# Optimization experiments

Hardware: AMD Instinct MI355X
Metric: run time of the kernel (lower is better)

## Reference

```python
import jax, jax.numpy as jnp
import numpy as np

B, S, T = 1024, 1024, 16


def setup_inputs() -> dict:
    key = jax.random.key(0)
    k1, k2, k3, k4, k5 = jax.random.split(key, 5)
    emissions = jax.random.normal(k1, (B, S, T), dtype=jnp.float32)
    tags = jax.random.randint(k2, (B, S), 0, T, dtype=jnp.int64)
    mask = jnp.ones((B, S), dtype=bool)
    # parameters (original uses uniform(-0.1, 0.1) init)
    transitions = jax.random.uniform(k3, (T, T), minval=-0.1, maxval=0.1, dtype=jnp.float32)
    start_transitions = jax.random.uniform(k4, (T,), minval=-0.1, maxval=0.1, dtype=jnp.float32)
    end_transitions = jax.random.uniform(k5, (T,), minval=-0.1, maxval=0.1, dtype=jnp.float32)
    return {
        "emissions": emissions,
        "tags": tags,
        "mask": mask,
        "transitions": transitions,
        "start_transitions": start_transitions,
        "end_transitions": end_transitions,
    }


def _forward_algorithm(emissions, mask, transitions, start_transitions, end_transitions):
    # emissions: [B,S,T], mask: [B,S] bool -> log partition [B]
    score0 = start_transitions + emissions[:, 0]  # [B,T]

    def step(score, xs):
        em_t, m_t = xs  # em_t: [B,T], m_t: [B]
        # next[b,i,j] = score[b,i] + transitions[i,j] + em_t[b,j]
        nxt = score[:, :, None] + transitions[None, :, :] + em_t[:, None, :]
        nxt = jax.nn.logsumexp(nxt, axis=1)  # over previous tag i
        score = jnp.where(m_t[:, None], nxt, score)
        return score, None

    em_rest = jnp.swapaxes(emissions[:, 1:], 0, 1)  # [S-1,B,T]
    m_rest = jnp.swapaxes(mask[:, 1:], 0, 1)        # [S-1,B]
    score, _ = jax.lax.scan(step, score0, (em_rest, m_rest))
    score = score + end_transitions
    return jax.nn.logsumexp(score, axis=1)


def _score_sentence(emissions, tags, mask, transitions, start_transitions, end_transitions):
    # gold-path score, vectorized over time. [B]
    bidx = jnp.arange(emissions.shape[0])
    score = start_transitions[tags[:, 0]] + emissions[:, 0][bidx, tags[:, 0]]
    # per-step emission scores [B,S]
    emit = jnp.take_along_axis(emissions, tags[:, :, None], axis=2)[:, :, 0]
    # NOTE: faithful to original: transitions[tags[t], tags[t-1]]
    trans = transitions[tags[:, 1:], tags[:, :-1]]  # [B,S-1]
    m = mask[:, 1:].astype(emissions.dtype)
    score = score + jnp.sum((emit[:, 1:] + trans) * m, axis=1)
    last_idx = jnp.sum(mask.astype(jnp.int32), axis=1) - 1  # [B]
    last_tags = jnp.take_along_axis(tags, last_idx[:, None].astype(tags.dtype), axis=1)[:, 0]
    score = score + end_transitions[last_tags]
    return score


def reference(emissions, tags, mask, transitions, start_transitions, end_transitions):
    emissions = emissions.astype(jnp.float32)
    gold = _score_sentence(emissions, tags, mask, transitions, start_transitions, end_transitions)
    logZ = _forward_algorithm(emissions, mask, transitions, start_transitions, end_transitions)
    nll = logZ - gold
    return jnp.mean(nll)
```

## Files before the change

kernel.cpp:

```cpp
#include <hip/hip_runtime.h>
#include <stdint.h>


#define BB 1024
#define SS 1024
#define TT 16
#define CC 16
#define LL 64
#define P1B (BB * CC / 4)

typedef float    f32x4 __attribute__((ext_vector_type(4)));
typedef int      i32x4 __attribute__((ext_vector_type(4)));
typedef short    s16x4 __attribute__((ext_vector_type(4)));
typedef uint32_t u32x2 __attribute__((ext_vector_type(2)));

__device__ __forceinline__ uint32_t pkt(float lo, float hi) {
    return __builtin_amdgcn_perm(__float_as_uint(hi), __float_as_uint(lo), 0x07060302u);
}
__device__ __forceinline__ s16x4 mk_frag(uint32_t lo, uint32_t hi) {
    u32x2 t; t.x = lo; t.y = hi;
    return __builtin_bit_cast(s16x4, t);
}

__global__ __launch_bounds__(256, 4) void fused1_kernel(
        const float* __restrict__ em,
        const float* __restrict__ trans,
        const int*   __restrict__ tags,
        const float* __restrict__ startt,
        const float* __restrict__ endt,
        float* __restrict__ mats,
        int*   __restrict__ scales,
        float* __restrict__ gold)
{
    __shared__ float xbuf[4][LL * TT];
    __shared__ int   sbuf[4][16];
    __shared__ float red[256];
    if (blockIdx.x < P1B) {
        const int wave = threadIdx.x >> 6;
        const int lane = threadIdx.x & 63;
        const int id   = blockIdx.x * 4 + wave;
        const int b    = id >> 4;
        const int c    = id & 15;
        const int q    = lane >> 4;
        const int m    = lane & 15;

        const float comp = 1.00390625f;
        const float a0 = __expf(trans[(4*q + 0) * TT + m]) * comp;
        const float a1 = __expf(trans[(4*q + 1) * TT + m]) * comp;
        const float a2 = __expf(trans[(4*q + 2) * TT + m]) * comp;
        const float a3 = __expf(trans[(4*q + 3) * TT + m]) * comp;
        const s16x4 afr = mk_frag(pkt(a0, a1), pkt(a2, a3));

        const float* ep = em + (size_t)b * SS * TT + (size_t)c * LL * TT + lane;
        float* xb = xbuf[wave];
        {
            float v[16];
            #pragma unroll
            for (int k = 0; k < 16; ++k) v[k] = ep[k * 64];
            #pragma unroll
            for (int k = 0; k < 16; ++k) xb[k * 64 + lane] = __expf(v[k]);
        }

        f32x4 sd0, sd1;
        sd0[0] = sd1[0] = (4*q + 0 == m) ? 1.f : 0.f;
        sd0[1] = sd1[1] = (4*q + 1 == m) ? 1.f : 0.f;
        sd0[2] = sd1[2] = (4*q + 2 == m) ? 1.f : 0.f;
        sd0[3] = sd1[3] = (4*q + 3 == m) ? 1.f : 0.f;
        const f32x4 zero = {0.f, 0.f, 0.f, 0.f};
        int sc0 = 0, sc1 = 0;
        const bool skip0 = (c == 0);

#define RESCALE(sd, sc) {                                                   \
        float mx = fmaxf(fmaxf(sd[0], sd[1]), fmaxf(sd[2], sd[3]));         \
        mx = fmaxf(mx, __shfl_xor(mx, 16, 64));                             \
        mx = fmaxf(mx, __shfl_xor(mx, 32, 64));                             \
        const int e_ = (int)(__float_as_uint(mx) >> 23) - 127;              \
        const float sf_ = __uint_as_float((uint32_t)(127 - e_) << 23);      \
        sd[0] *= sf_; sd[1] *= sf_; sd[2] *= sf_; sd[3] *= sf_;             \
        sc += e_; }

        const float* xlo = xb + 4 * q;
        const float* xhi = xb + 512 + 4 * q;
        f32x4 x0 = *(const f32x4*)(xlo);
        f32x4 x1 = *(const f32x4*)(xhi);

        #pragma unroll
        for (int i = 0; i < 32; ++i) {
            f32x4 nx0, nx1;
            if (i < 31) {
                nx0 = *(const f32x4*)(xlo + (i + 1) * TT);
                nx1 = *(const f32x4*)(xhi + (i + 1) * TT);
            }
            if (!(skip0 && i == 0)) {
                const s16x4 b0 = mk_frag(pkt(sd0[0], sd0[1]), pkt(sd0[2], sd0[3]));
                const f32x4 d0 = __builtin_amdgcn_mfma_f32_16x16x16bf16_1k(afr, b0, zero, 0, 0, 0);
                sd0 = d0 * x0;
            }
            {
                const s16x4 b1 = mk_frag(pkt(sd1[0], sd1[1]), pkt(sd1[2], sd1[3]));
                const f32x4 d1 = __builtin_amdgcn_mfma_f32_16x16x16bf16_1k(afr, b1, zero, 0, 0, 0);
                sd1 = d1 * x1;
            }
            x0 = nx0; x1 = nx1;
            if ((i & 7) == 7) { RESCALE(sd0, sc0); RESCALE(sd1, sc1); }
        }

        xb[(4*q + 0) * TT + m] = sd1[0];
        xb[(4*q + 1) * TT + m] = sd1[1];
        xb[(4*q + 2) * TT + m] = sd1[2];
        xb[(4*q + 3) * TT + m] = sd1[3];
        if (q == 0) sbuf[wave][m] = sc1;
        const f32x4 at  = *(const f32x4*)(xb + m * TT + 4 * q);
        const i32x4 sh  = *(const i32x4*)(sbuf[wave] + 4 * q);
        int shimax = sc1;
        #pragma unroll
        for (int s = 1; s < 16; s <<= 1) shimax = max(shimax, __shfl_xor(shimax, s, 64));
        const float r0 = ldexpf(sd0[0], sh.x - shimax);
        const float r1 = ldexpf(sd0[1], sh.y - shimax);
        const float r2 = ldexpf(sd0[2], sh.z - shimax);
        const float r3 = ldexpf(sd0[3], sh.w - shimax);
        const s16x4 bfm = mk_frag(pkt(r0, r1), pkt(r2, r3));
        const s16x4 afm = mk_frag(pkt(at.x, at.y), pkt(at.z, at.w));
        f32x4 sd = __builtin_amdgcn_mfma_f32_16x16x16bf16_1k(afm, bfm, zero, 0, 0, 0);
        int sc = sc0 + shimax;
        RESCALE(sd, sc);
#undef RESCALE

        float* mp = mats + (size_t)id * 256;
        mp[(4*q + 0) * TT + m] = sd[0];
        mp[(4*q + 1) * TT + m] = sd[1];
        mp[(4*q + 2) * TT + m] = sd[2];
        mp[(4*q + 3) * TT + m] = sd[3];
        if (q == 0) scales[id * 16 + m] = sc;
    } else {
        const int b = blockIdx.x - P1B, tid = threadIdx.x;
        float local = 0.f;
        for (int t = tid; t < SS; t += 256) {
            const int tg = tags[b * SS + t];
            float v = em[(size_t)(b * SS + t) * TT + tg];
            if (t > 0) v += trans[tg * TT + tags[b * SS + t - 1]];
            else       v += startt[tg];
            if (t == SS - 1) v += endt[tg];
            local += v;
        }
        red[tid] = local; __syncthreads();
        for (int s = 128; s > 0; s >>= 1) { if (tid < s) red[tid] += red[tid + s]; __syncthreads(); }
        if (tid == 0) gold[b] = red[0];
    }
}

__global__ __launch_bounds__(256) void combine_kernel(
        const float* __restrict__ em,
        const float* __restrict__ startt,
        const float* __restrict__ endt,
        const float* __restrict__ mats,
        const int*   __restrict__ scales,
        const float* __restrict__ gold,
        float* __restrict__ out)
{
    const int wave = threadIdx.x >> 6;
    const int lane = threadIdx.x & 63;
    const int b    = blockIdx.x * 4 + wave;
    const int q    = lane >> 4;
    const int m    = lane & 15;

    const float* m0 = mats + (size_t)(b * CC) * 256;
    f32x4 d;
    d[0] = m0[(4*q + 0) * TT + m];
    d[1] = m0[(4*q + 1) * TT + m];
    d[2] = m0[(4*q + 2) * TT + m];
    d[3] = m0[(4*q + 3) * TT + m];
    int sig = scales[(b * CC) * 16 + m];
    int gam = 0;
    const f32x4 zero = {0.f, 0.f, 0.f, 0.f};

    #pragma unroll 4
    for (int c = 1; c < CC; ++c) {
        const int idc = b * CC + c;
        const f32x4 a = *(const f32x4*)(mats + (size_t)idc * 256 + m * TT + 4 * q);
        const i32x4 s = *(const i32x4*)(scales + idc * 16 + 4 * q);
        int sm = max(max(s.x, s.y), max(s.z, s.w));
        sm = max(sm, __shfl_xor(sm, 16, 64));
        sm = max(sm, __shfl_xor(sm, 32, 64));
        const float r0 = ldexpf(d[0], s.x - sm);
        const float r1 = ldexpf(d[1], s.y - sm);
        const float r2 = ldexpf(d[2], s.z - sm);
        const float r3 = ldexpf(d[3], s.w - sm);
        const s16x4 bfr = mk_frag(pkt(r0, r1), pkt(r2, r3));
        const s16x4 afr = mk_frag(pkt(a.x, a.y), pkt(a.z, a.w));
        d = __builtin_amdgcn_mfma_f32_16x16x16bf16_1k(afr, bfr, zero, 0, 0, 0);
        gam += sm;
        float mx = fmaxf(fmaxf(d[0], d[1]), fmaxf(d[2], d[3]));
        mx = fmaxf(mx, __shfl_xor(mx, 16, 64));
        mx = fmaxf(mx, __shfl_xor(mx, 32, 64));
        const int e = (int)(__float_as_uint(mx) >> 23) - 127;
        const float sf = __uint_as_float((uint32_t)(127 - e) << 23);
        d[0] *= sf; d[1] *= sf; d[2] *= sf; d[3] *= sf;
        sig += e;
    }

    const float s0 = startt[m] + em[(size_t)b * SS * TT + m];
    float mx0 = s0;
    #pragma unroll
    for (int s = 1; s < 16; s <<= 1) mx0 = fmaxf(mx0, __shfl_xor(mx0, s, 64));
    const float u0n = __expf(s0 - mx0);

    int sigmax = sig;
    #pragma unroll
    for (int s = 1; s < 16; s <<= 1) sigmax = max(sigmax, __shfl_xor(sigmax, s, 64));
    const float w = ldexpf(u0n, sig - sigmax);

    f32x4 v;
    v[0] = d[0] * w; v[1] = d[1] * w; v[2] = d[2] * w; v[3] = d[3] * w;
    #pragma unroll
    for (int s = 1; s < 16; s <<= 1) {
        v[0] += __shfl_xor(v[0], s, 64);
        v[1] += __shfl_xor(v[1], s, 64);
        v[2] += __shfl_xor(v[2], s, 64);
        v[3] += __shfl_xor(v[3], s, 64);
    }
    const f32x4 ee = *(const f32x4*)(endt + 4 * q);
    float z = __expf(ee.x) * v[0] + __expf(ee.y) * v[1]
            + __expf(ee.z) * v[2] + __expf(ee.w) * v[3];
    z += __shfl_xor(z, 16, 64);
    z += __shfl_xor(z, 32, 64);

    if (lane == 0) {
        const float logZ = mx0 + 0.69314718055994531f * (float)(gam + sigmax) + __logf(z);
        atomicAdd(out, (logZ - gold[b]) * (1.0f / BB));
    }
}

extern "C" void kernel_launch(void* const* d_in, const int* in_sizes, int n_in,
                              void* d_out, int out_size, void* d_ws, size_t ws_size,
                              hipStream_t stream) {
    const float* em     = (const float*)d_in[0];
    const int*   tags   = (const int*)  d_in[1];
    const float* trans  = (const float*)d_in[3];
    const float* startt = (const float*)d_in[4];
    const float* endt   = (const float*)d_in[5];
    float* out = (float*)d_out;

    float* mats   = (float*)d_ws;
    int*   scales = (int*)((char*)d_ws + (size_t)BB * CC * 256 * 4);
    float* gold   = (float*)((char*)scales + (size_t)BB * CC * 16 * 4);

    hipMemsetAsync(out, 0, sizeof(float), stream);
    fused1_kernel<<<P1B + BB, 256, 0, stream>>>(em, trans, tags, startt, endt, mats, scales, gold);
    combine_kernel<<<BB / 4, 256, 0, stream>>>(em, startt, endt, mats, scales, gold, out);
}
```

Measured before the change: 141.3 us.

## Fold emission scaling into MFMA A-operand and drop memset launch

Each step now scales the exp-transition matrix by the emission value, built as a packed MFMA A fragment, instead of multiplying the MFMA output by the emission vector. The shared-memory emission buffer is transposed into a padded per-tag row layout (stride 68) so each lane reads four timesteps in one vector load. The output zeroing memset is replaced by a store inside the first kernel, saving one launch. This adds packing work per step and rounds the scaled transition matrix to bf16, which changes precision behavior. Zeroing out inside the first kernel relies on it finishing before combine_kernel's atomics, which stream order provides.

```diff
diff --git a/kernel.cpp b/kernel.cpp
--- a/kernel.cpp
+++ b/kernel.cpp
@@ -7,9 +7,11 @@
 #define TT 16
 #define CC 16
 #define LL 64
+#define XS 68
 #define P1B (BB * CC / 4)
 
 typedef float    f32x4 __attribute__((ext_vector_type(4)));
+typedef float    f32x2 __attribute__((ext_vector_type(2)));
 typedef int      i32x4 __attribute__((ext_vector_type(4)));
 typedef short    s16x4 __attribute__((ext_vector_type(4)));
 typedef uint32_t u32x2 __attribute__((ext_vector_type(2)));
@@ -30,9 +32,10 @@
         const float* __restrict__ endt,
         float* __restrict__ mats,
         int*   __restrict__ scales,
-        float* __restrict__ gold)
+        float* __restrict__ gold,
+        float* __restrict__ out)
 {
-    __shared__ float xbuf[4][LL * TT];
+    __shared__ float xbuf[4][TT * XS];
     __shared__ int   sbuf[4][16];
     __shared__ float red[256];
     if (blockIdx.x < P1B) {
@@ -45,11 +48,11 @@
         const int m    = lane & 15;
 
         const float comp = 1.00390625f;
-        const float a0 = __expf(trans[(4*q + 0) * TT + m]) * comp;
-        const float a1 = __expf(trans[(4*q + 1) * TT + m]) * comp;
-        const float a2 = __expf(trans[(4*q + 2) * TT + m]) * comp;
-        const float a3 = __expf(trans[(4*q + 3) * TT + m]) * comp;
-        const s16x4 afr = mk_frag(pkt(a0, a1), pkt(a2, a3));
+        f32x2 e01, e23;
+        e01.x = __expf(trans[(4*q + 0) * TT + m]) * comp;
+        e01.y = __expf(trans[(4*q + 1) * TT + m]) * comp;
+        e23.x = __expf(trans[(4*q + 2) * TT + m]) * comp;
+        e23.y = __expf(trans[(4*q + 3) * TT + m]) * comp;
 
         const float* ep = em + (size_t)b * SS * TT + (size_t)c * LL * TT + lane;
         float* xb = xbuf[wave];
@@ -58,7 +61,7 @@
             #pragma unroll
             for (int k = 0; k < 16; ++k) v[k] = ep[k * 64];
             #pragma unroll
-            for (int k = 0; k < 16; ++k) xb[k * 64 + lane] = __expf(v[k]);
+            for (int k = 0; k < 16; ++k) xb[m * XS + 4 * k + q] = __expf(v[k]);
         }
 
         f32x4 sd0, sd1;
@@ -79,30 +82,32 @@
         sd[0] *= sf_; sd[1] *= sf_; sd[2] *= sf_; sd[3] *= sf_;             \
         sc += e_; }
 
-        const float* xlo = xb + 4 * q;
-        const float* xhi = xb + 512 + 4 * q;
-        f32x4 x0 = *(const f32x4*)(xlo);
-        f32x4 x1 = *(const f32x4*)(xhi);
+#define STEP(sd, xm) {                                                      \
+        f32x2 xx; xx.x = (xm); xx.y = (xm);                                 \
+        const f32x2 a01 = xx * e01;                                         \
+        const f32x2 a23 = xx * e23;                                         \
+        const s16x4 afr = mk_frag(pkt(a01.x, a01.y), pkt(a23.x, a23.y));    \
+        const s16x4 bfr = mk_frag(pkt(sd[0], sd[1]), pkt(sd[2], sd[3]));    \
+        sd = __builtin_amdgcn_mfma_f32_16x16x16bf16_1k(afr, bfr, zero, 0, 0, 0); }
+
+        const float* xrow = xb + m * XS;
+        f32x4 cx0 = *(const f32x4*)(xrow);
+        f32x4 cx1 = *(const f32x4*)(xrow + 32);
 
         #pragma unroll
-        for (int i = 0; i < 32; ++i) {
+        for (int g = 0; g < 8; ++g) {
             f32x4 nx0, nx1;
-            if (i < 31) {
-                nx0 = *(const f32x4*)(xlo + (i + 1) * TT);
-                nx1 = *(const f32x4*)(xhi + (i + 1) * TT);
+            if (g < 7) {
+                nx0 = *(const f32x4*)(xrow + 4 * (g + 1));
+                nx1 = *(const f32x4*)(xrow + 32 + 4 * (g + 1));
             }
-            if (!(skip0 && i == 0)) {
-                const s16x4 b0 = mk_frag(pkt(sd0[0], sd0[1]), pkt(sd0[2], sd0[3]));
-                const f32x4 d0 = __builtin_amdgcn_mfma_f32_16x16x16bf16_1k(afr, b0, zero, 0, 0, 0);
-                sd0 = d0 * x0;
+            #pragma unroll
+            for (int i = 0; i < 4; ++i) {
+                if (!(skip0 && g == 0 && i == 0)) STEP(sd0, cx0[i]);
+                STEP(sd1, cx1[i]);
             }
-            {
-                const s16x4 b1 = mk_frag(pkt(sd1[0], sd1[1]), pkt(sd1[2], sd1[3]));
-                const f32x4 d1 = __builtin_amdgcn_mfma_f32_16x16x16bf16_1k(afr, b1, zero, 0, 0, 0);
-                sd1 = d1 * x1;
-            }
-            x0 = nx0; x1 = nx1;
-            if ((i & 7) == 7) { RESCALE(sd0, sc0); RESCALE(sd1, sc1); }
+            if (g & 1) { RESCALE(sd0, sc0); RESCALE(sd1, sc1); }
+            cx0 = nx0; cx1 = nx1;
         }
 
         xb[(4*q + 0) * TT + m] = sd1[0];
@@ -125,6 +130,7 @@
         int sc = sc0 + shimax;
         RESCALE(sd, sc);
 #undef RESCALE
+#undef STEP
 
         float* mp = mats + (size_t)id * 256;
         mp[(4*q + 0) * TT + m] = sd[0];
@@ -134,6 +140,7 @@
         if (q == 0) scales[id * 16 + m] = sc;
     } else {
         const int b = blockIdx.x - P1B, tid = threadIdx.x;
+        if (b == 0 && tid == 0) out[0] = 0.f;
         float local = 0.f;
         for (int t = tid; t < SS; t += 256) {
             const int tg = tags[b * SS + t];
@@ -245,7 +252,6 @@
     int*   scales = (int*)((char*)d_ws + (size_t)BB * CC * 256 * 4);
     float* gold   = (float*)((char*)scales + (size_t)BB * CC * 16 * 4);
 
-    hipMemsetAsync(out, 0, sizeof(float), stream);
-    fused1_kernel<<<P1B + BB, 256, 0, stream>>>(em, trans, tags, startt, endt, mats, scales, gold);
+    fused1_kernel<<<P1B + BB, 256, 0, stream>>>(em, trans, tags, startt, endt, mats, scales, gold, out);
     combine_kernel<<<BB / 4, 256, 0, stream>>>(em, startt, endt, mats, scales, gold, out);
 }
```

Measured after the change: 138.3 us. -2.1%, faster.
